# Kernel tuning notes

Measured on AMD Instinct MI355X. Metric: run time of the kernel, lower is better.

The kernel has to match this reference:

```python
import jax, jax.numpy as jnp
import numpy as np

H = 512      # hidden_channels
NP = 20000   # politician nodes
NS = 10000   # stock nodes
E = 400000   # edges per relation / trade edges
FP = 64      # raw politician feature dim
FS = 64      # raw stock feature dim
NC = 3       # num_classes


def setup_inputs() -> dict:
    key = jax.random.key(0)
    ks = iter(jax.random.split(key, 40))

    def rn(shape, s=0.05):
        return (jax.random.normal(next(ks), shape, jnp.float32) * s).astype(jnp.float32)

    inp = {}
    inp["x_pol"] = rn((NP, FP), 1.0)
    inp["x_stock"] = rn((NS, FS), 1.0)
    inp["trade_edge_attr"] = rn((E, 2), 1.0)
    # input projections (torch Linear: y = x @ W + b)
    inp["Wp"] = rn((FP, H)); inp["bp"] = rn((H,))
    inp["Ws"] = rn((FS, H)); inp["bs"] = rn((H,))
    # SAGEConv params: Wl/bl act on mean-aggregated neighbors, Wr on root (no bias)
    for layer in ("c1", "c2"):
        for rel in ("ps", "sp"):
            inp[f"{layer}_{rel}_Wl"] = rn((H, H))
            inp[f"{layer}_{rel}_bl"] = rn((H,))
            inp[f"{layer}_{rel}_Wr"] = rn((H, H))
    # decoder MLP
    inp["d1_W"] = rn((2 * H + 2, H)); inp["d1_b"] = rn((H,))
    inp["d2_W"] = rn((H, NC)); inp["d2_b"] = rn((NC,))
    # edge indices
    inp["edge_ps_src"] = jax.random.randint(next(ks), (E,), 0, NP, jnp.int64 if jax.config.jax_enable_x64 else jnp.int32)
    inp["edge_ps_dst"] = jax.random.randint(next(ks), (E,), 0, NS, jnp.int32)
    inp["edge_sp_src"] = jax.random.randint(next(ks), (E,), 0, NS, jnp.int32)
    inp["edge_sp_dst"] = jax.random.randint(next(ks), (E,), 0, NP, jnp.int32)
    inp["trade_row"] = jax.random.randint(next(ks), (E,), 0, NP, jnp.int32)
    inp["trade_col"] = jax.random.randint(next(ks), (E,), 0, NS, jnp.int32)
    inp["edge_ps_src"] = inp["edge_ps_src"].astype(jnp.int32)
    return inp


def sage_conv(x_src, x_dst, src, dst, Wl, bl, Wr, n_dst):
    # PyG SAGEConv (aggr='mean', root_weight=True, normalize=False):
    # out = lin_l(mean_{j->i} x_j) + lin_r(x_i)
    msg = x_src[src]                                            # [E, H] gather
    agg = jax.ops.segment_sum(msg, dst, num_segments=n_dst)     # [n_dst, H]
    cnt = jax.ops.segment_sum(jnp.ones((src.shape[0], 1), x_src.dtype), dst, num_segments=n_dst)
    mean = agg / jnp.maximum(cnt, 1.0)
    return mean @ Wl + bl + x_dst @ Wr


def reference(x_pol, x_stock, trade_edge_attr,
              Wp, bp, Ws, bs,
              c1_ps_Wl, c1_ps_bl, c1_ps_Wr, c1_sp_Wl, c1_sp_bl, c1_sp_Wr,
              c2_ps_Wl, c2_ps_bl, c2_ps_Wr, c2_sp_Wl, c2_sp_bl, c2_sp_Wr,
              d1_W, d1_b, d2_W, d2_b,
              edge_ps_src, edge_ps_dst, edge_sp_src, edge_sp_dst,
              trade_row, trade_col):
    # per-node-type input projection + relu
    hp = jax.nn.relu(x_pol @ Wp + bp)      # [NP, H]
    hs = jax.nn.relu(x_stock @ Ws + bs)    # [NS, H]
    # conv1 (HeteroConv sum: each node type is dst of exactly one relation)
    hs1 = sage_conv(hp, hs, edge_ps_src, edge_ps_dst, c1_ps_Wl, c1_ps_bl, c1_ps_Wr, hs.shape[0])
    hp1 = sage_conv(hs, hp, edge_sp_src, edge_sp_dst, c1_sp_Wl, c1_sp_bl, c1_sp_Wr, hp.shape[0])
    hp1, hs1 = jax.nn.relu(hp1), jax.nn.relu(hs1)
    # conv2
    hs2 = sage_conv(hp1, hs1, edge_ps_src, edge_ps_dst, c2_ps_Wl, c2_ps_bl, c2_ps_Wr, hs1.shape[0])
    hp2 = sage_conv(hs1, hp1, edge_sp_src, edge_sp_dst, c2_sp_Wl, c2_sp_bl, c2_sp_Wr, hp1.shape[0])
    hp2, hs2 = jax.nn.relu(hp2), jax.nn.relu(hs2)
    # edge decoder (Dropout is identity at inference)
    feat = jnp.concatenate([hp2[trade_row], hs2[trade_col], trade_edge_attr], axis=-1)  # [E, 2H+2]
    h = jax.nn.relu(feat @ d1_W + d1_b)
    return h @ d2_W + d2_b  # [E, NC]
```

## Files before the change

kernel.cpp:

```cpp
#include <hip/hip_runtime.h>
#include <hip/hip_bf16.h>

typedef unsigned short u16;
typedef unsigned int u32;
typedef __attribute__((ext_vector_type(8))) short short8;
typedef __attribute__((ext_vector_type(4))) float f32x4;
typedef __attribute__((ext_vector_type(2))) float f32x2;

#define NP 20000
#define NS 10000
#define NE 400000
#define H  512
#define FDIM 64
#define ECHUNK 16

__device__ __forceinline__ float bl16(u32 w){ return __uint_as_float(w << 16); }
__device__ __forceinline__ float bh16(u32 w){ return __uint_as_float(w & 0xffff0000u); }
__device__ __forceinline__ u16 f2bf(float f){
  u32 u = __float_as_uint(f);
  u32 r = u + 0x7fffu + ((u >> 16) & 1u);
  return (u16)(r >> 16);
}
__device__ __forceinline__ u32 pack2(float a, float b){
  return (u32)f2bf(a) | ((u32)f2bf(b) << 16);
}
__device__ __forceinline__ void gload16(const void* g, void* l){
  __builtin_amdgcn_global_load_lds((const __attribute__((address_space(1))) u32*)g,
                                   (__attribute__((address_space(3))) u32*)l, 16, 0, 0);
}
__device__ __forceinline__ f32x2 pk_fma(f32x2 a, f32x2 b, f32x2 c){
  f32x2 d;
  asm("v_pk_fma_f32 %0, %1, %2, %3" : "=v"(d) : "v"(a), "v"(b), "v"(c));
  return d;
}
__device__ __forceinline__ f32x2 pk_add(f32x2 a, f32x2 b){
  f32x2 d;
  asm("v_pk_add_f32 %0, %1, %2" : "=v"(d) : "v"(a), "v"(b));
  return d;
}

__global__ __launch_bounds__(256) void proj_kernel(const float* __restrict__ X, const float* __restrict__ W,
                                                   const float* __restrict__ b, u16* __restrict__ Y, int n)
{
  __shared__ float xs[8][FDIM];
  int tid = threadIdx.x;
  int m0 = blockIdx.x * 8;
  {
    int r = tid >> 6, c = tid & 63;
    int m = m0 + r;
    xs[r][c] = (m < n) ? X[(size_t)m*FDIM + c] : 0.f;
    m = m0 + r + 4;
    xs[r+4][c] = (m < n) ? X[(size_t)m*FDIM + c] : 0.f;
  }
  __syncthreads();
  float acc[8][2] = {};
  int c0 = tid, c1 = tid + 256;
  for (int k = 0; k < FDIM; ++k){
    float w0 = W[k*H + c0];
    float w1 = W[k*H + c1];
    #pragma unroll
    for (int r = 0; r < 8; ++r){
      float xv = xs[r][k];
      acc[r][0] = fmaf(xv, w0, acc[r][0]);
      acc[r][1] = fmaf(xv, w1, acc[r][1]);
    }
  }
  float b0 = b[c0], b1 = b[c1];
  #pragma unroll
  for (int r = 0; r < 8; ++r){
    int m = m0 + r;
    if (m < n){
      Y[(size_t)m*H + c0] = f2bf(fmaxf(acc[r][0] + b0, 0.f));
      Y[(size_t)m*H + c1] = f2bf(fmaxf(acc[r][1] + b1, 0.f));
    }
  }
}

struct TPair { const float* src; u16* dst; };
struct TArgs { TPair m[10]; };

__global__ __launch_bounds__(256) void wtrans_kernel(TArgs args)
{
  __shared__ float lds[32][33];
  int mat = blockIdx.z;
  const float* __restrict__ src = args.m[mat].src;
  u16* __restrict__ dst = args.m[mat].dst;
  int k0 = blockIdx.y << 5, n0 = blockIdx.x << 5;
  int t = threadIdx.x;
  int r = t >> 3, c4 = (t & 7) << 2;
  float4 v = *(const float4*)(src + (size_t)(k0 + r)*H + n0 + c4);
  lds[r][c4+0] = v.x; lds[r][c4+1] = v.y; lds[r][c4+2] = v.z; lds[r][c4+3] = v.w;
  __syncthreads();
  uint2 o;
  o.x = pack2(lds[c4+0][r], lds[c4+1][r]);
  o.y = pack2(lds[c4+2][r], lds[c4+3][r]);
  *(uint2*)(dst + (size_t)(n0 + r)*H + k0 + c4) = o;
}

__global__ void hist_kernel(const int* __restrict__ ps_dst, const int* __restrict__ sp_dst,
                            const int* __restrict__ trow,
                            int* __restrict__ cnt_s, int* __restrict__ cnt_p, int* __restrict__ cnt_t)
{
  int e = blockIdx.x * blockDim.x + threadIdx.x;
  if (e < NE){
    atomicAdd(&cnt_s[ps_dst[e]], 1);
    atomicAdd(&cnt_p[sp_dst[e]], 1);
    atomicAdd(&cnt_t[trow[e]], 1);
  }
}

__device__ void scan_one(int* cnt, int n, int* rowptr)
{
  __shared__ int wsum[16];
  __shared__ int carry_s;
  int tid = threadIdx.x;
  int lane = tid & 63, wv = tid >> 6;
  if (tid == 0) carry_s = 0;
  for (int base = 0; base < n; base += 1024){
    __syncthreads();
    int i = base + tid;
    int v = (i < n) ? cnt[i] : 0;
    int x = v;
    #pragma unroll
    for (int off = 1; off < 64; off <<= 1){
      int t = __shfl_up(x, off);
      if (lane >= off) x += t;
    }
    if (lane == 63) wsum[wv] = x;
    __syncthreads();
    if (wv == 0 && lane < 16){
      int y = wsum[lane];
      #pragma unroll
      for (int off = 1; off < 16; off <<= 1){
        int t = __shfl_up(y, off, 16);
        if (lane >= off) y += t;
      }
      wsum[lane] = y;
    }
    __syncthreads();
    int woff = (wv > 0) ? wsum[wv-1] : 0;
    int cb = carry_s;
    int excl = cb + woff + x - v;
    if (i < n){ rowptr[i] = excl; cnt[i] = excl; }
    __syncthreads();
    if (tid == 1023) carry_s = cb + woff + x;
  }
  __syncthreads();
  if (tid == 0) rowptr[n] = carry_s;
}

__global__ __launch_bounds__(1024) void scan3_kernel(int* c0, int n0, int* r0,
                                                     int* c1, int n1, int* r1,
                                                     int* c2, int n2, int* r2)
{
  if (blockIdx.x == 0) scan_one(c0, n0, r0);
  else if (blockIdx.x == 1) scan_one(c1, n1, r1);
  else scan_one(c2, n2, r2);
}

__global__ void scatter_kernel(const int* __restrict__ ps_src, const int* __restrict__ ps_dst,
                               const int* __restrict__ sp_src, const int* __restrict__ sp_dst,
                               const int* __restrict__ trow, const int* __restrict__ tcol,
                               const float* __restrict__ attr,
                               int* __restrict__ cur_s, int* __restrict__ cur_p, int* __restrict__ cur_t,
                               int* __restrict__ sorted_ps, int* __restrict__ sorted_sp,
                               int4* __restrict__ meta_t, float2* __restrict__ attr_t)
{
  int e = blockIdx.x * blockDim.x + threadIdx.x;
  if (e < NE){
    int pos = atomicAdd(&cur_s[ps_dst[e]], 1);
    sorted_ps[pos] = ps_src[e];
    int pos2 = atomicAdd(&cur_p[sp_dst[e]], 1);
    sorted_sp[pos2] = sp_src[e];
    int r = trow[e];
    int pos3 = atomicAdd(&cur_t[r], 1);
    meta_t[pos3] = make_int4(e, r, tcol[e], 0);
    attr_t[pos3] = make_float2(attr[2*e], attr[2*e+1]);
  }
}

__global__ __launch_bounds__(256) void agg2_kernel(
    const u16* __restrict__ X0, const int* __restrict__ rp0, const int* __restrict__ s0,
    u16* __restrict__ M0, int n0,
    const u16* __restrict__ X1, const int* __restrict__ rp1, const int* __restrict__ s1,
    u16* __restrict__ M1, int n1)
{
  int wid = (blockIdx.x << 2) + (threadIdx.x >> 6);
  int lane = threadIdx.x & 63;
  const u16* X; const int* rp; const int* ss; u16* M; int row;
  if (wid < n0){ X = X0; rp = rp0; ss = s0; M = M0; row = wid; }
  else if (wid < n0 + n1){ X = X1; rp = rp1; ss = s1; M = M1; row = wid - n0; }
  else return;
  int beg = rp[row], end = rp[row + 1];
  f32x2 ac0 = {0,0}, ac1 = {0,0}, ac2 = {0,0}, ac3 = {0,0};
  int j0 = lane << 3;
#define ACCP(v) { ac0 = pk_add(ac0, (f32x2){bl16(v.x), bh16(v.x)}); \
                  ac1 = pk_add(ac1, (f32x2){bl16(v.y), bh16(v.y)}); \
                  ac2 = pk_add(ac2, (f32x2){bl16(v.z), bh16(v.z)}); \
                  ac3 = pk_add(ac3, (f32x2){bl16(v.w), bh16(v.w)}); }
  int i = beg;
  for (; i + 8 <= end; i += 8){
    int sa = ss[i+0], sb = ss[i+1], sc = ss[i+2], sd = ss[i+3];
    int se = ss[i+4], sf = ss[i+5], sg = ss[i+6], sh = ss[i+7];
    uint4 v0 = *(const uint4*)(X + (size_t)sa*H + j0);
    uint4 v1 = *(const uint4*)(X + (size_t)sb*H + j0);
    uint4 v2 = *(const uint4*)(X + (size_t)sc*H + j0);
    uint4 v3 = *(const uint4*)(X + (size_t)sd*H + j0);
    uint4 v4 = *(const uint4*)(X + (size_t)se*H + j0);
    uint4 v5 = *(const uint4*)(X + (size_t)sf*H + j0);
    uint4 v6 = *(const uint4*)(X + (size_t)sg*H + j0);
    uint4 v7 = *(const uint4*)(X + (size_t)sh*H + j0);
    ACCP(v0); ACCP(v1); ACCP(v2); ACCP(v3);
    ACCP(v4); ACCP(v5); ACCP(v6); ACCP(v7);
  }
  for (; i + 2 <= end; i += 2){
    int sa = ss[i], sb = ss[i+1];
    uint4 v0 = *(const uint4*)(X + (size_t)sa*H + j0);
    uint4 v1 = *(const uint4*)(X + (size_t)sb*H + j0);
    ACCP(v0); ACCP(v1);
  }
  if (i < end){
    int sa = ss[i];
    uint4 v0 = *(const uint4*)(X + (size_t)sa*H + j0);
    ACCP(v0);
  }
#undef ACCP
  float inv = 1.f / (float)max(end - beg, 1);
  uint4 o;
  o.x = pack2(ac0.x*inv, ac0.y*inv);
  o.y = pack2(ac1.x*inv, ac1.y*inv);
  o.z = pack2(ac2.x*inv, ac2.y*inv);
  o.w = pack2(ac3.x*inv, ac3.y*inv);
  *(uint4*)(M + (size_t)row*H + j0) = o;
}

struct GemmProb {
  const u16* A1; const u16* W1t; const u16* A2; const u16* W2t;
  const float* bias; u16* C; int nrows; int relu;
};

__global__ __launch_bounds__(512) void gemm_mfma256(GemmProb Pa, GemmProb Pb)
{
  GemmProb P = blockIdx.z ? Pb : Pa;
  int m0 = blockIdx.y << 8, n0 = blockIdx.x << 8;
  if (m0 >= P.nrows) return;

  __shared__ u16 lds[2][2][256*64];
  int t = threadIdx.x;
  int w = t >> 6, l = t & 63;
  int wm = w >> 2, wn = w & 3;
  int lr = l & 15, lg = l >> 4;

  f32x4 acc[8][4];
  #pragma unroll
  for (int i = 0; i < 8; ++i)
    #pragma unroll
    for (int j = 0; j < 4; ++j)
      acc[i][j] = (f32x4){0.f, 0.f, 0.f, 0.f};

  const u16* Asrc0 = P.A1; const u16* Asrc1 = P.A2;
  const u16* Wsrc0 = P.W1t; const u16* Wsrc1 = P.W2t;
  int NT = P.A2 ? 16 : 8;

  auto STAGE = [&](int kt, int buf){
    const u16* Ap = (kt < 8) ? Asrc0 : Asrc1;
    const u16* Wp = (kt < 8) ? Wsrc0 : Wsrc1;
    int k0 = (kt & 7) << 6;
    char* AsB = (char*)lds[buf][0];
    char* BsB = (char*)lds[buf][1];
    #pragma unroll
    for (int i = 0; i < 4; ++i){
      int c = i*512 + t;
      int row = c >> 3, p = c & 7;
      int k8 = p ^ (row & 7);
      gload16(Ap + (size_t)(m0 + row)*H + k0 + k8*8, AsB + c*16);
      gload16(Wp + (size_t)(n0 + row)*H + k0 + k8*8, BsB + c*16);
    }
  };

  STAGE(0, 0);
  for (int kt = 0; kt < NT; ++kt){
    int cur = kt & 1;
    if (kt + 1 < NT){
      STAGE(kt + 1, cur ^ 1);
      asm volatile("s_waitcnt vmcnt(8)" ::: "memory");
    } else {
      asm volatile("s_waitcnt vmcnt(0)" ::: "memory");
    }
    __builtin_amdgcn_sched_barrier(0);
    __builtin_amdgcn_s_barrier();
    __builtin_amdgcn_sched_barrier(0);
    const char* AsB = (const char*)lds[cur][0];
    const char* BsB = (const char*)lds[cur][1];
    #pragma unroll
    for (int ph = 0; ph < 4; ++ph){
      const int mh = ph & 1, ks = ph >> 1;
      short8 a[4], b[4];
      int kc = (ks << 2) + lg;
      #pragma unroll
      for (int i = 0; i < 4; ++i){
        int r = (wm << 7) + (mh << 6) + (i << 4) + lr;
        a[i] = *(const short8*)(AsB + r*128 + ((kc ^ (r & 7)) << 4));
      }
      #pragma unroll
      for (int nf = 0; nf < 4; ++nf){
        int r = (wn << 6) + (nf << 4) + lr;
        b[nf] = *(const short8*)(BsB + r*128 + ((kc ^ (r & 7)) << 4));
      }
      __builtin_amdgcn_s_setprio(1);
      #pragma unroll
      for (int i = 0; i < 4; ++i)
        #pragma unroll
        for (int nf = 0; nf < 4; ++nf)
          acc[(mh << 2) + i][nf] =
            __builtin_amdgcn_mfma_f32_16x16x32_bf16(a[i], b[nf], acc[(mh << 2) + i][nf], 0, 0, 0);
      __builtin_amdgcn_s_setprio(0);
    }
    asm volatile("" ::: "memory");
    __builtin_amdgcn_s_barrier();
    __builtin_amdgcn_sched_barrier(0);
  }

  float bvn[4];
  #pragma unroll
  for (int nf = 0; nf < 4; ++nf)
    bvn[nf] = P.bias ? P.bias[n0 + (wn << 6) + (nf << 4) + lr] : 0.f;
  #pragma unroll
  for (int mf = 0; mf < 8; ++mf){
    #pragma unroll
    for (int j = 0; j < 4; ++j){
      int m = m0 + (wm << 7) + (mf << 4) + (lg << 2) + j;
      if (m < P.nrows){
        #pragma unroll
        for (int nf = 0; nf < 4; ++nf){
          float v = acc[mf][nf][j] + bvn[nf];
          if (P.relu) v = fmaxf(v, 0.f);
          P.C[(size_t)m*H + n0 + (wn << 6) + (nf << 4) + lr] = f2bf(v);
        }
      }
    }
  }
}

__global__ __launch_bounds__(256) void edge_chunk_kernel(
    const u16* __restrict__ Adec, const u16* __restrict__ Bdec,
    const float* __restrict__ d1W, const float* __restrict__ d2W,
    const float* __restrict__ d2b,
    const int4* __restrict__ meta_t, const float2* __restrict__ attr_t,
    float* __restrict__ out)
{
  int lane = threadIdx.x & 63;
  int ch = (blockIdx.x << 2) + (threadIdx.x >> 6);
  int base = ch * ECHUNK;
  if (base >= NE) return;
  int j0 = lane << 3;

  f32x2 w1a2[4], w1b2[4], w20[4], w21[4], w22[4];
  #pragma unroll
  for (int q = 0; q < 4; ++q){
    int c = j0 + 2*q;
    w1a2[q] = (f32x2){ d1W[(size_t)1024*H + c], d1W[(size_t)1024*H + c + 1] };
    w1b2[q] = (f32x2){ d1W[(size_t)1025*H + c], d1W[(size_t)1025*H + c + 1] };
    w20[q]  = (f32x2){ d2W[c*3 + 0], d2W[(c+1)*3 + 0] };
    w21[q]  = (f32x2){ d2W[c*3 + 1], d2W[(c+1)*3 + 1] };
    w22[q]  = (f32x2){ d2W[c*3 + 2], d2W[(c+1)*3 + 2] };
  }
  float ob0 = d2b[0], ob1 = d2b[1], ob2 = d2b[2];

  int4 mv = make_int4(0,0,0,0);
  float2 av = make_float2(0.f,0.f);
  if (lane < ECHUNK){ mv = meta_t[base + lane]; av = attr_t[base + lane]; }

  int cached_r = -1;
  f32x2 fa2[4];
  auto loadA = [&](int r){
    cached_r = r;
    uint4 va = *(const uint4*)(Adec + (size_t)r*H + j0);
    fa2[0] = (f32x2){bl16(va.x), bh16(va.x)};
    fa2[1] = (f32x2){bl16(va.y), bh16(va.y)};
    fa2[2] = (f32x2){bl16(va.z), bh16(va.z)};
    fa2[3] = (f32x2){bl16(va.w), bh16(va.w)};
  };

  uint4 vb[4];
  #pragma unroll
  for (int d = 0; d < 4; ++d){
    int c = __shfl(mv.z, d);
    vb[d] = *(const uint4*)(Bdec + (size_t)c*H + j0);
  }

  #pragma unroll
  for (int i = 0; i < ECHUNK; ++i){
    uint4 vc = vb[i & 3];
    if (i + 4 < ECHUNK){
      int cn = __shfl(mv.z, i + 4);
      vb[i & 3] = *(const uint4*)(Bdec + (size_t)cn*H + j0);
    }
    int e  = __shfl(mv.x, i);
    int r  = __shfl(mv.y, i);
    float a0 = __shfl(av.x, i);
    float a1 = __shfl(av.y, i);
    if (r != cached_r) loadA(r);

    f32x2 a0v = (f32x2){a0, a0}, a1v = (f32x2){a1, a1};
    f32x2 fb[4] = { (f32x2){bl16(vc.x), bh16(vc.x)}, (f32x2){bl16(vc.y), bh16(vc.y)},
                    (f32x2){bl16(vc.z), bh16(vc.z)}, (f32x2){bl16(vc.w), bh16(vc.w)} };
    f32x2 s0 = {0,0}, s1 = {0,0}, s2 = {0,0};
    #pragma unroll
    for (int q = 0; q < 4; ++q){
      f32x2 u = pk_add(fa2[q], fb[q]);
      u = pk_fma(a0v, w1a2[q], u);
      u = pk_fma(a1v, w1b2[q], u);
      u.x = fmaxf(u.x, 0.f); u.y = fmaxf(u.y, 0.f);
      s0 = pk_fma(u, w20[q], s0);
      s1 = pk_fma(u, w21[q], s1);
      s2 = pk_fma(u, w22[q], s2);
    }
    float r0 = s0.x + s0.y, r1 = s1.x + s1.y, r2 = s2.x + s2.y;
    #pragma unroll
    for (int off = 32; off > 0; off >>= 1){
      r0 += __shfl_xor(r0, off);
      r1 += __shfl_xor(r1, off);
      r2 += __shfl_xor(r2, off);
    }
    if (lane == 0){
      out[(size_t)e*3 + 0] = r0 + ob0;
      out[(size_t)e*3 + 1] = r1 + ob1;
      out[(size_t)e*3 + 2] = r2 + ob2;
    }
  }
}

extern "C" void kernel_launch(void* const* d_in, const int* in_sizes, int n_in,
                              void* d_out, int out_size, void* d_ws, size_t ws_size,
                              hipStream_t stream)
{
  const float* x_pol    = (const float*)d_in[0];
  const float* x_stock  = (const float*)d_in[1];
  const float* attr     = (const float*)d_in[2];
  const float* Wp       = (const float*)d_in[3];
  const float* bp       = (const float*)d_in[4];
  const float* Wst      = (const float*)d_in[5];
  const float* bst      = (const float*)d_in[6];
  const float* c1_ps_Wl = (const float*)d_in[7];
  const float* c1_ps_bl = (const float*)d_in[8];
  const float* c1_ps_Wr = (const float*)d_in[9];
  const float* c1_sp_Wl = (const float*)d_in[10];
  const float* c1_sp_bl = (const float*)d_in[11];
  const float* c1_sp_Wr = (const float*)d_in[12];
  const float* c2_ps_Wl = (const float*)d_in[13];
  const float* c2_ps_bl = (const float*)d_in[14];
  const float* c2_ps_Wr = (const float*)d_in[15];
  const float* c2_sp_Wl = (const float*)d_in[16];
  const float* c2_sp_bl = (const float*)d_in[17];
  const float* c2_sp_Wr = (const float*)d_in[18];
  const float* d1W      = (const float*)d_in[19];
  const float* d1b      = (const float*)d_in[20];
  const float* d2W      = (const float*)d_in[21];
  const float* d2b      = (const float*)d_in[22];
  const int* ps_src     = (const int*)d_in[23];
  const int* ps_dst     = (const int*)d_in[24];
  const int* sp_src     = (const int*)d_in[25];
  const int* sp_dst     = (const int*)d_in[26];
  const int* trow       = (const int*)d_in[27];
  const int* tcol       = (const int*)d_in[28];
  float* out = (float*)d_out;

  char* ws = (char*)d_ws;
  size_t off = 0;
  auto alloc = [&](size_t bytes)->char*{
    char* p = ws + off;
    off += (bytes + 255) & ~(size_t)255;
    return p;
  };
  u16* P0 = (u16*)alloc((size_t)NP*H*2);
  u16* P1 = (u16*)alloc((size_t)NP*H*2);
  u16* S0 = (u16*)alloc((size_t)NS*H*2);
  u16* S1 = (u16*)alloc((size_t)NS*H*2);
  u16* MP = (u16*)alloc((size_t)NP*H*2);
  u16* MS = (u16*)alloc((size_t)NS*H*2);
  u16* Wt[10];
  for (int i = 0; i < 10; ++i) Wt[i] = (u16*)alloc((size_t)H*H*2);
  int* cnt_s    = (int*)alloc((size_t)NS*4);
  int* cnt_p    = (int*)alloc((size_t)NP*4);
  int* cnt_t    = (int*)alloc((size_t)NP*4);
  int* rowptr_s = (int*)alloc((size_t)(NS+1)*4);
  int* rowptr_p = (int*)alloc((size_t)(NP+1)*4);
  int* rowptr_t = (int*)alloc((size_t)(NP+1)*4);
  int* sorted_ps = (int*)alloc((size_t)NE*4);
  int* sorted_sp = (int*)alloc((size_t)NE*4);
  int4* meta_t   = (int4*)alloc((size_t)NE*16);
  float2* attr_t = (float2*)alloc((size_t)NE*8);
  alloc((size_t)256*H*2);

  TArgs ta;
  ta.m[0] = {c1_ps_Wl, Wt[0]}; ta.m[1] = {c1_ps_Wr, Wt[1]};
  ta.m[2] = {c1_sp_Wl, Wt[2]}; ta.m[3] = {c1_sp_Wr, Wt[3]};
  ta.m[4] = {c2_ps_Wl, Wt[4]}; ta.m[5] = {c2_ps_Wr, Wt[5]};
  ta.m[6] = {c2_sp_Wl, Wt[6]}; ta.m[7] = {c2_sp_Wr, Wt[7]};
  ta.m[8] = {d1W, Wt[8]};
  ta.m[9] = {d1W + (size_t)512*H, Wt[9]};
  wtrans_kernel<<<dim3(16,16,10), 256, 0, stream>>>(ta);

  hipMemsetAsync(cnt_s, 0, (size_t)NS*4, stream);
  hipMemsetAsync(cnt_p, 0, (size_t)NP*4, stream);
  hipMemsetAsync(cnt_t, 0, (size_t)NP*4, stream);
  hist_kernel<<<(NE+255)/256, 256, 0, stream>>>(ps_dst, sp_dst, trow, cnt_s, cnt_p, cnt_t);
  scan3_kernel<<<3, 1024, 0, stream>>>(cnt_s, NS, rowptr_s, cnt_p, NP, rowptr_p, cnt_t, NP, rowptr_t);
  scatter_kernel<<<(NE+255)/256, 256, 0, stream>>>(ps_src, ps_dst, sp_src, sp_dst, trow, tcol, attr,
                                                   cnt_s, cnt_p, cnt_t,
                                                   sorted_ps, sorted_sp, meta_t, attr_t);

  proj_kernel<<<(NP+7)/8, 256, 0, stream>>>(x_pol, Wp, bp, P0, NP);
  proj_kernel<<<(NS+7)/8, 256, 0, stream>>>(x_stock, Wst, bst, S0, NS);

  int aggGrid = (NS + NP + 3) / 4;
  int gRows = (NP + 255) / 256;

  agg2_kernel<<<aggGrid, 256, 0, stream>>>(P0, rowptr_s, sorted_ps, MS, NS,
                                           S0, rowptr_p, sorted_sp, MP, NP);
  {
    GemmProb a = {MS, Wt[0], S0, Wt[1], c1_ps_bl, S1, NS, 1};
    GemmProb b = {MP, Wt[2], P0, Wt[3], c1_sp_bl, P1, NP, 1};
    gemm_mfma256<<<dim3(2, gRows, 2), 512, 0, stream>>>(a, b);
  }

  agg2_kernel<<<aggGrid, 256, 0, stream>>>(P1, rowptr_s, sorted_ps, MS, NS,
                                           S1, rowptr_p, sorted_sp, MP, NP);
  {
    GemmProb a = {MS, Wt[4], S1, Wt[5], c2_ps_bl, S0, NS, 1};
    GemmProb b = {MP, Wt[6], P1, Wt[7], c2_sp_bl, P0, NP, 1};
    gemm_mfma256<<<dim3(2, gRows, 2), 512, 0, stream>>>(a, b);
  }

  {
    GemmProb a = {P0, Wt[8], nullptr, nullptr, d1b, MP, NP, 0};
    GemmProb b = {S0, Wt[9], nullptr, nullptr, nullptr, MS, NS, 0};
    gemm_mfma256<<<dim3(2, gRows, 2), 512, 0, stream>>>(a, b);
  }

  int nchunks = NE / ECHUNK;
  edge_chunk_kernel<<<(nchunks + 3) / 4, 256, 0, stream>>>(MP, MS, d1W, d2W, d2b,
                                                           meta_t, attr_t, out);
}
```

Measured before the change: 601.5 us.

## Compute edge decoder second layer with MFMA over 16-edge tiles

```diff
diff --git a/kernel.cpp b/kernel.cpp
--- a/kernel.cpp
+++ b/kernel.cpp
@@ -95,6 +95,22 @@
   o.x = pack2(lds[c4+0][r], lds[c4+1][r]);
   o.y = pack2(lds[c4+2][r], lds[c4+3][r]);
   *(uint2*)(dst + (size_t)(n0 + r)*H + k0 + c4) = o;
+}
+
+__global__ __launch_bounds__(256) void w2frag_kernel(const float* __restrict__ d2W, uint4* __restrict__ w2f)
+{
+  int tid = blockIdx.x*256 + threadIdx.x;
+  int l = tid & 63;
+  int col = l & 15, g = l >> 4;
+  int k = (tid >> 6)*32 + g*8;
+  float v[8];
+  #pragma unroll
+  for (int j = 0; j < 8; ++j)
+    v[j] = (col < 3) ? d2W[(size_t)(k+j)*3 + col] : 0.f;
+  uint4 o;
+  o.x = pack2(v[0], v[1]); o.y = pack2(v[2], v[3]);
+  o.z = pack2(v[4], v[5]); o.w = pack2(v[6], v[7]);
+  w2f[tid] = o;
 }
 
 __global__ void hist_kernel(const int* __restrict__ ps_dst, const int* __restrict__ sp_dst,
@@ -342,92 +358,84 @@
   }
 }
 
-__global__ __launch_bounds__(256) void edge_chunk_kernel(
+__global__ __launch_bounds__(256) void edge_mfma_kernel(
     const u16* __restrict__ Adec, const u16* __restrict__ Bdec,
-    const float* __restrict__ d1W, const float* __restrict__ d2W,
+    const uint4* __restrict__ w2f, const float* __restrict__ d1W,
     const float* __restrict__ d2b,
     const int4* __restrict__ meta_t, const float2* __restrict__ attr_t,
     float* __restrict__ out)
 {
-  int lane = threadIdx.x & 63;
-  int ch = (blockIdx.x << 2) + (threadIdx.x >> 6);
+  __shared__ uint4 w2s[16*64];
+  __shared__ float w1s[2][H];
+  int t = threadIdx.x;
+  #pragma unroll
+  for (int i = 0; i < 4; ++i)
+    w2s[i*256 + t] = w2f[i*256 + t];
+  ((float4*)w1s)[t] = ((const float4*)(d1W + (size_t)1024*H))[t];
+  __syncthreads();
+
+  int lane = t & 63;
+  int ch = (blockIdx.x << 2) + (t >> 6);
   int base = ch * ECHUNK;
   if (base >= NE) return;
-  int j0 = lane << 3;
-
-  f32x2 w1a2[4], w1b2[4], w20[4], w21[4], w22[4];
-  #pragma unroll
-  for (int q = 0; q < 4; ++q){
-    int c = j0 + 2*q;
-    w1a2[q] = (f32x2){ d1W[(size_t)1024*H + c], d1W[(size_t)1024*H + c + 1] };
-    w1b2[q] = (f32x2){ d1W[(size_t)1025*H + c], d1W[(size_t)1025*H + c + 1] };
-    w20[q]  = (f32x2){ d2W[c*3 + 0], d2W[(c+1)*3 + 0] };
-    w21[q]  = (f32x2){ d2W[c*3 + 1], d2W[(c+1)*3 + 1] };
-    w22[q]  = (f32x2){ d2W[c*3 + 2], d2W[(c+1)*3 + 2] };
-  }
-  float ob0 = d2b[0], ob1 = d2b[1], ob2 = d2b[2];
+  int er = lane & 15, g = lane >> 4;
 
   int4 mv = make_int4(0,0,0,0);
   float2 av = make_float2(0.f,0.f);
   if (lane < ECHUNK){ mv = meta_t[base + lane]; av = attr_t[base + lane]; }
-
-  int cached_r = -1;
-  f32x2 fa2[4];
-  auto loadA = [&](int r){
-    cached_r = r;
-    uint4 va = *(const uint4*)(Adec + (size_t)r*H + j0);
-    fa2[0] = (f32x2){bl16(va.x), bh16(va.x)};
-    fa2[1] = (f32x2){bl16(va.y), bh16(va.y)};
-    fa2[2] = (f32x2){bl16(va.z), bh16(va.z)};
-    fa2[3] = (f32x2){bl16(va.w), bh16(va.w)};
-  };
-
-  uint4 vb[4];
-  #pragma unroll
-  for (int d = 0; d < 4; ++d){
-    int c = __shfl(mv.z, d);
-    vb[d] = *(const uint4*)(Bdec + (size_t)c*H + j0);
-  }
-
-  #pragma unroll
-  for (int i = 0; i < ECHUNK; ++i){
-    uint4 vc = vb[i & 3];
-    if (i + 4 < ECHUNK){
-      int cn = __shfl(mv.z, i + 4);
-      vb[i & 3] = *(const uint4*)(Bdec + (size_t)cn*H + j0);
-    }
-    int e  = __shfl(mv.x, i);
-    int r  = __shfl(mv.y, i);
-    float a0 = __shfl(av.x, i);
-    float a1 = __shfl(av.y, i);
-    if (r != cached_r) loadA(r);
-
-    f32x2 a0v = (f32x2){a0, a0}, a1v = (f32x2){a1, a1};
-    f32x2 fb[4] = { (f32x2){bl16(vc.x), bh16(vc.x)}, (f32x2){bl16(vc.y), bh16(vc.y)},
-                    (f32x2){bl16(vc.z), bh16(vc.z)}, (f32x2){bl16(vc.w), bh16(vc.w)} };
-    f32x2 s0 = {0,0}, s1 = {0,0}, s2 = {0,0};
-    #pragma unroll
-    for (int q = 0; q < 4; ++q){
-      f32x2 u = pk_add(fa2[q], fb[q]);
-      u = pk_fma(a0v, w1a2[q], u);
-      u = pk_fma(a1v, w1b2[q], u);
-      u.x = fmaxf(u.x, 0.f); u.y = fmaxf(u.y, 0.f);
-      s0 = pk_fma(u, w20[q], s0);
-      s1 = pk_fma(u, w21[q], s1);
-      s2 = pk_fma(u, w22[q], s2);
-    }
-    float r0 = s0.x + s0.y, r1 = s1.x + s1.y, r2 = s2.x + s2.y;
-    #pragma unroll
-    for (int off = 32; off > 0; off >>= 1){
-      r0 += __shfl_xor(r0, off);
-      r1 += __shfl_xor(r1, off);
-      r2 += __shfl_xor(r2, off);
-    }
-    if (lane == 0){
-      out[(size_t)e*3 + 0] = r0 + ob0;
-      out[(size_t)e*3 + 1] = r1 + ob1;
-      out[(size_t)e*3 + 2] = r2 + ob2;
-    }
+  int p = __shfl(mv.y, er);
+  int c = __shfl(mv.z, er);
+  float a0 = __shfl(av.x, er);
+  float a1 = __shfl(av.y, er);
+  f32x2 a0v = {a0, a0}, a1v = {a1, a1};
+
+  const u16* Arow = Adec + (size_t)p*H + g*8;
+  const u16* Brow = Bdec + (size_t)c*H + g*8;
+
+  f32x4 acc = {0.f, 0.f, 0.f, 0.f};
+  #pragma unroll
+  for (int ks = 0; ks < 16; ++ks){
+    uint4 va = *(const uint4*)(Arow + ks*32);
+    uint4 vb = *(const uint4*)(Brow + ks*32);
+    const float* wa = &w1s[0][ks*32 + g*8];
+    const float* wb = &w1s[1][ks*32 + g*8];
+    float4 wa0 = *(const float4*)(wa);
+    float4 wa1 = *(const float4*)(wa + 4);
+    float4 wb0 = *(const float4*)(wb);
+    float4 wb1 = *(const float4*)(wb + 4);
+    f32x2 h0 = pk_add((f32x2){bl16(va.x), bh16(va.x)}, (f32x2){bl16(vb.x), bh16(vb.x)});
+    f32x2 h1 = pk_add((f32x2){bl16(va.y), bh16(va.y)}, (f32x2){bl16(vb.y), bh16(vb.y)});
+    f32x2 h2 = pk_add((f32x2){bl16(va.z), bh16(va.z)}, (f32x2){bl16(vb.z), bh16(vb.z)});
+    f32x2 h3 = pk_add((f32x2){bl16(va.w), bh16(va.w)}, (f32x2){bl16(vb.w), bh16(vb.w)});
+    h0 = pk_fma(a0v, (f32x2){wa0.x, wa0.y}, h0);
+    h1 = pk_fma(a0v, (f32x2){wa0.z, wa0.w}, h1);
+    h2 = pk_fma(a0v, (f32x2){wa1.x, wa1.y}, h2);
+    h3 = pk_fma(a0v, (f32x2){wa1.z, wa1.w}, h3);
+    h0 = pk_fma(a1v, (f32x2){wb0.x, wb0.y}, h0);
+    h1 = pk_fma(a1v, (f32x2){wb0.z, wb0.w}, h1);
+    h2 = pk_fma(a1v, (f32x2){wb1.x, wb1.y}, h2);
+    h3 = pk_fma(a1v, (f32x2){wb1.z, wb1.w}, h3);
+    uint4 hh;
+    hh.x = pack2(fmaxf(h0.x, 0.f), fmaxf(h0.y, 0.f));
+    hh.y = pack2(fmaxf(h1.x, 0.f), fmaxf(h1.y, 0.f));
+    hh.z = pack2(fmaxf(h2.x, 0.f), fmaxf(h2.y, 0.f));
+    hh.w = pack2(fmaxf(h3.x, 0.f), fmaxf(h3.y, 0.f));
+    short8 pa = __builtin_bit_cast(short8, hh);
+    short8 pb = __builtin_bit_cast(short8, w2s[ks*64 + lane]);
+    acc = __builtin_amdgcn_mfma_f32_16x16x32_bf16(pa, pb, acc, 0, 0, 0);
+  }
+
+  int ebc[4];
+  #pragma unroll
+  for (int j = 0; j < 4; ++j)
+    ebc[j] = __shfl(mv.x, (g << 2) + j);
+
+  int col = lane & 15;
+  if (col < 3){
+    float ob = d2b[col];
+    #pragma unroll
+    for (int j = 0; j < 4; ++j)
+      out[(size_t)ebc[j]*3 + col] = acc[j] + ob;
   }
 }
 
@@ -491,6 +499,7 @@
   int* sorted_sp = (int*)alloc((size_t)NE*4);
   int4* meta_t   = (int4*)alloc((size_t)NE*16);
   float2* attr_t = (float2*)alloc((size_t)NE*8);
+  uint4* w2f     = (uint4*)alloc((size_t)16*64*16);
   alloc((size_t)256*H*2);
 
   TArgs ta;
@@ -501,6 +510,7 @@
   ta.m[8] = {d1W, Wt[8]};
   ta.m[9] = {d1W + (size_t)512*H, Wt[9]};
   wtrans_kernel<<<dim3(16,16,10), 256, 0, stream>>>(ta);
+  w2frag_kernel<<<4, 256, 0, stream>>>(d2W, w2f);
 
   hipMemsetAsync(cnt_s, 0, (size_t)NS*4, stream);
   hipMemsetAsync(cnt_p, 0, (size_t)NP*4, stream);
@@ -540,6 +550,6 @@
   }
 
   int nchunks = NE / ECHUNK;
-  edge_chunk_kernel<<<(nchunks + 3) / 4, 256, 0, stream>>>(MP, MS, d1W, d2W, d2b,
-                                                           meta_t, attr_t, out);
-}
+  edge_mfma_kernel<<<(nchunks + 3) / 4, 256, 0, stream>>>(MP, MS, w2f, d1W, d2b,
+                                                          meta_t, attr_t, out);
+}
```

Measured after the change: 580.4 us. 1.04x faster.
